# Optimization experiments

Hardware: AMD Instinct MI355X
Metric: run time of the kernel (lower is better)

Reference implementation:

```python
import jax, jax.numpy as jnp
import numpy as np


def setup_inputs() -> dict:
    key = jax.random.key(0)
    ks = jax.random.split(key, 6)
    b, t, k, h = 2, 2048, 256, 8
    s = 1.0 / np.sqrt(k)
    return {
        "x": jax.random.normal(ks[0], (b, t, k), dtype=jnp.float32),
        "Wq": jax.random.normal(ks[1], (k, k * h), dtype=jnp.float32) * s,
        "Wk": jax.random.normal(ks[2], (k, k * h), dtype=jnp.float32) * s,
        "Wv": jax.random.normal(ks[3], (k, k * h), dtype=jnp.float32) * s,
        "Wu": jax.random.normal(ks[4], (k * h, k), dtype=jnp.float32) * (1.0 / np.sqrt(k * h)),
        "bu": jnp.zeros((k,), dtype=jnp.float32),
    }


def reference(x, Wq, Wk, Wv, Wu, bu):
    b, t, k = x.shape
    h = Wq.shape[1] // k
    scale = k ** (-0.25)
    # projections -> [b, t, h, k] -> [b, h, t, k]
    q = (x @ Wq).reshape(b, t, h, k).transpose(0, 2, 1, 3) * scale
    kk = (x @ Wk).reshape(b, t, h, k).transpose(0, 2, 1, 3) * scale
    v = (x @ Wv).reshape(b, t, h, k).transpose(0, 2, 1, 3)
    dot = jnp.einsum('bhqk,bhsk->bhqs', q, kk)  # [b,h,t,t]
    attn = jax.nn.softmax(dot, axis=-1)
    out = jnp.einsum('bhqs,bhsk->bhqk', attn, v)  # [b,h,t,k]
    out = out.transpose(0, 2, 1, 3).reshape(b, t, h * k)
    return out @ Wu + bu
```

## Files before the change

kernel.cpp:

```cpp
#include <hip/hip_runtime.h>

using bf16x8   = __bf16 __attribute__((ext_vector_type(8)));
using floatx4  = float __attribute__((ext_vector_type(4)));
using floatx16 = float __attribute__((ext_vector_type(16)));

static __device__ __forceinline__ unsigned short f2b(float x) {
  unsigned u = __builtin_bit_cast(unsigned, x);
  u = (u + 0x7fffu + ((u >> 16) & 1u)) >> 16;
  return (unsigned short)u;
}

static __device__ __forceinline__ void gl_lds16(const unsigned short* g, unsigned short* l) {
  __builtin_amdgcn_global_load_lds((const __attribute__((address_space(1))) void*)g,
                                   (__attribute__((address_space(3))) void*)l, 16, 0, 0);
}

__global__ __launch_bounds__(256) void prep_kernel(const float* __restrict__ x,
                                                   const float* __restrict__ Wq,
                                                   const float* __restrict__ Wk,
                                                   const float* __restrict__ Wv,
                                                   const float* __restrict__ Wu,
                                                   unsigned short* __restrict__ xb,
                                                   unsigned short* __restrict__ wqkt,
                                                   unsigned short* __restrict__ wvt,
                                                   unsigned short* __restrict__ wut) {
  int bx = blockIdx.x;
  if (bx < 1024) {
    int i = (bx * 256 + threadIdx.x) * 4;
    float4 v = *(const float4*)(x + i);
    unsigned long long p = (unsigned long long)f2b(v.x) |
                           ((unsigned long long)f2b(v.y) << 16) |
                           ((unsigned long long)f2b(v.z) << 32) |
                           ((unsigned long long)f2b(v.w) << 48);
    *(unsigned long long*)(xb + i) = p;
    return;
  }
  __shared__ unsigned short T[64][65];
  const float* src;
  unsigned short* dst;
  int R, C, tile;
  if (bx < 1152)      { src = Wq; dst = wqkt;          R = 256;  C = 2048; tile = bx - 1024; }
  else if (bx < 1280) { src = Wk; dst = wqkt + 524288; R = 256;  C = 2048; tile = bx - 1152; }
  else if (bx < 1408) { src = Wv; dst = wvt;           R = 256;  C = 2048; tile = bx - 1280; }
  else                { src = Wu; dst = wut;           R = 2048; C = 256;  tile = bx - 1408; }
  int ctiles = C >> 6;
  int cx = tile % ctiles, ry = tile / ctiles;
  int r0 = ry * 64, c0 = cx * 64;
  int t = threadIdx.x;
#pragma unroll
  for (int i = 0; i < 16; ++i) {
    int idx = i * 256 + t;
    int r = idx >> 6, c = idx & 63;
    T[r][c] = f2b(src[(size_t)(r0 + r) * C + c0 + c]);
  }
  __syncthreads();
#pragma unroll
  for (int i = 0; i < 16; ++i) {
    int idx = i * 256 + t;
    int c = idx >> 6, r = idx & 63;
    dst[(size_t)(c0 + c) * R + r0 + r] = T[r][c];
  }
}

__global__ __launch_bounds__(256) void proj_kernel(const unsigned short* __restrict__ A,
                                                   const unsigned short* __restrict__ Bt,
                                                   unsigned short* __restrict__ qkb,
                                                   unsigned short* __restrict__ vtb) {
  __shared__ __align__(16) unsigned short SMEM[128 * 136];
  unsigned short* As = SMEM;
  unsigned short* Bs = SMEM + 4096;
  const int Kt = 256;
  int tid = threadIdx.x, lane = tid & 63, w = tid >> 6;
  int m16 = lane & 15, quad = lane >> 4;
  int wr = w & 1, wc = w >> 1;
  int m0 = blockIdx.y * 128, n0 = blockIdx.x * 128;
  int srow0 = w * 32 + (lane >> 2);
  int schunk = (lane & 3) ^ ((lane >> 2) & 3);
  floatx4 acc[4][4] = {};
  for (int k0 = 0; k0 < Kt; k0 += 32) {
    __syncthreads();
#pragma unroll
    for (int j = 0; j < 2; ++j) {
      int r = srow0 + j * 16;
      gl_lds16(A + (size_t)(m0 + r) * Kt + k0 + schunk * 8, &As[(w * 32 + j * 16) * 32]);
      gl_lds16(Bt + (size_t)(n0 + r) * Kt + k0 + schunk * 8, &Bs[(w * 32 + j * 16) * 32]);
    }
    __syncthreads();
    int sw = (quad ^ (m16 & 3)) * 8;
    bf16x8 af[4], bfr[4];
#pragma unroll
    for (int i = 0; i < 4; ++i) {
      af[i]  = *(const bf16x8*)(&As[(wr * 64 + i * 16 + m16) * 32 + sw]);
      bfr[i] = *(const bf16x8*)(&Bs[(wc * 64 + i * 16 + m16) * 32 + sw]);
    }
#pragma unroll
    for (int i = 0; i < 4; ++i)
#pragma unroll
      for (int jn = 0; jn < 4; ++jn)
        acc[i][jn] = __builtin_amdgcn_mfma_f32_16x16x32_bf16(af[i], bfr[jn], acc[i][jn], 0, 0, 0);
  }
  if (n0 < 4096) {
#pragma unroll
    for (int i = 0; i < 4; ++i)
#pragma unroll
      for (int jn = 0; jn < 4; ++jn)
#pragma unroll
        for (int r = 0; r < 4; ++r) {
          int m = m0 + wr * 64 + i * 16 + quad * 4 + r;
          int n = n0 + wc * 64 + jn * 16 + m16;
          qkb[(size_t)m * 4096 + n] = f2b(acc[i][jn][r]);
        }
  } else {
    __syncthreads();
    unsigned short* Vt = SMEM;
#pragma unroll
    for (int i = 0; i < 4; ++i)
#pragma unroll
      for (int jn = 0; jn < 4; ++jn)
#pragma unroll
        for (int r = 0; r < 4; ++r) {
          int nn = wc * 64 + jn * 16 + m16;
          int mm = wr * 64 + i * 16 + quad * 4 + r;
          Vt[nn * 136 + mm] = f2b(acc[i][jn][r]);
        }
    __syncthreads();
    int bb = m0 >> 11, t0 = m0 & 2047;
#pragma unroll
    for (int i2 = 0; i2 < 8; ++i2) {
      int idx = i2 * 256 + tid;
      int nn = idx >> 4;
      int mc = (idx & 15) * 8;
      uint4 v = *(const uint4*)(&Vt[nn * 136 + mc]);
      *(uint4*)(&vtb[((size_t)(bb * 2048 + n0 - 4096 + nn)) * 2048 + t0 + mc]) = v;
    }
  }
}

__global__ __launch_bounds__(256) void out_kernel(const unsigned short* __restrict__ A,
                                                  const unsigned short* __restrict__ Bt,
                                                  float* __restrict__ Cout,
                                                  const float* __restrict__ bias) {
  __shared__ unsigned short As[64 * 128];
  __shared__ unsigned short Bs[64 * 128];
  const int Kt = 2048;
  int tid = threadIdx.x, lane = tid & 63, w = tid >> 6;
  int m16 = lane & 15, quad = lane >> 4;
  int m0 = blockIdx.y * 64, n0 = blockIdx.x * 64;
  int srow_i = lane >> 4;
  int spos = lane & 15;
  int rsw = m16 & 7;
  floatx4 acc[4] = {};
  for (int k0 = 0; k0 < Kt; k0 += 128) {
    __syncthreads();
#pragma unroll
    for (int j = 0; j < 4; ++j) {
      int r = w * 16 + j * 4 + srow_i;
      gl_lds16(A + (size_t)(m0 + r) * Kt + k0 + ((spos ^ (r & 7)) * 8), &As[(w * 16 + j * 4) * 128]);
      gl_lds16(Bt + (size_t)(n0 + r) * Kt + k0 + ((spos ^ (r & 7)) * 8), &Bs[(w * 16 + j * 4) * 128]);
    }
    __syncthreads();
    bf16x8 af[4];
#pragma unroll
    for (int kk = 0; kk < 4; ++kk)
      af[kk] = *(const bf16x8*)(&As[(w * 16 + m16) * 128 + (((kk * 4 + quad) ^ rsw) * 8)]);
#pragma unroll
    for (int nt = 0; nt < 4; ++nt)
#pragma unroll
      for (int kk = 0; kk < 4; ++kk) {
        bf16x8 bfv = *(const bf16x8*)(&Bs[(nt * 16 + m16) * 128 + (((kk * 4 + quad) ^ rsw) * 8)]);
        acc[nt] = __builtin_amdgcn_mfma_f32_16x16x32_bf16(af[kk], bfv, acc[nt], 0, 0, 0);
      }
  }
#pragma unroll
  for (int nt = 0; nt < 4; ++nt)
#pragma unroll
    for (int r = 0; r < 4; ++r) {
      int m = m0 + w * 16 + quad * 4 + r;
      int n = n0 + nt * 16 + m16;
      Cout[(size_t)m * 256 + n] = acc[nt][r] + bias[n];
    }
}

__global__ __launch_bounds__(512, 2) void attn_kernel(const unsigned short* __restrict__ qk,
                                                      const unsigned short* __restrict__ vt,
                                                      unsigned short* __restrict__ ao) {
  __shared__ __align__(16) unsigned char SM[150016];
  unsigned short* KsBuf = (unsigned short*)SM;
  unsigned short* VsBuf = (unsigned short*)(SM + 65536);
  float* lsh = (float*)(SM + 149504);
  int tid = threadIdx.x, lane = tid & 63, w = tid >> 6;
  int c32 = lane & 31, hi = lane >> 5;
  int qg = w & 3, u = w >> 2;
  unsigned short* Pw = (unsigned short*)(SM + 131072) + w * 1152;
  int id = blockIdx.x;
  int xcd = id & 7, j = id >> 3;
  int bh = xcd + 8 * (j & 1);
  int q0 = (j >> 1) * 128;
  int b = bh >> 3, h = bh & 7;

  bf16x8 qf[16];
  const unsigned short* qrow =
      qk + (size_t)(b * 2048 + q0 + qg * 32 + c32) * 4096 + h * 256 + hi * 8;
#pragma unroll
  for (int kk = 0; kk < 16; ++kk) qf[kk] = *(const bf16x8*)(qrow + kk * 16);

  floatx16 O[8] = {};
  float lacc = 0.f;

  const unsigned short* kbase = qk + (size_t)b * 2048 * 4096 + 2048 + h * 256;
  const unsigned short* vbase = vt + (size_t)bh * 256 * 2048;

  int krow_i = lane >> 5, kpos = lane & 31;
  int vrow_i = lane >> 3, vpos = lane & 7;
  int ksw = c32 & 7;

#pragma unroll
  for (int i = 0; i < 4; ++i) {
    int kr = i * 2 + krow_i;
    gl_lds16(kbase + (size_t)(w * 8 + kr) * 4096 + ((kpos ^ (kr & 7)) * 8),
             KsBuf + (w * 8 + i * 2) * 256);
    int vr = i * 8 + vrow_i;
    gl_lds16(vbase + (size_t)(w * 32 + vr) * 2048 + ((vpos ^ vrow_i) * 8),
             VsBuf + (w * 32 + i * 8) * 64);
  }

  for (int st = 0; st < 32; ++st) {
    int cur = st & 1;
    unsigned short* Kc = KsBuf + cur * 16384;
    unsigned short* Vc = VsBuf + cur * 16384;
    __syncthreads();
    if (st < 31) {
      int s0 = (st + 1) * 64;
      unsigned short* kd = KsBuf + (1 - cur) * 16384;
      unsigned short* vd = VsBuf + (1 - cur) * 16384;
#pragma unroll
      for (int i = 0; i < 4; ++i) {
        int kr = i * 2 + krow_i;
        gl_lds16(kbase + (size_t)(s0 + w * 8 + kr) * 4096 + ((kpos ^ (kr & 7)) * 8),
                 kd + (w * 8 + i * 2) * 256);
        int vr = i * 8 + vrow_i;
        gl_lds16(vbase + (size_t)(w * 32 + vr) * 2048 + s0 + ((vpos ^ vrow_i) * 8),
                 vd + (w * 32 + i * 8) * 64);
      }
    }

    floatx16 s = {};
    const unsigned short* krl = Kc + (u * 32 + c32) * 256;
#pragma unroll
    for (int kk = 0; kk < 16; ++kk) {
      bf16x8 kf = *(const bf16x8*)(krl + (((kk * 2 + hi) ^ ksw) * 8));
      s = __builtin_amdgcn_mfma_f32_32x32x16_bf16(kf, qf[kk], s, 0, 0, 0);
    }
    float lsum = 0.f;
#pragma unroll
    for (int i = 0; i < 16; ++i) {
      float p = __expf(s[i] * 0.0625f);
      lsum += p;
      int sl = (i & 3) + 8 * (i >> 2) + 4 * hi;
      Pw[c32 * 36 + sl] = f2b(p);
    }
    lacc += lsum;
    bf16x8 paf[2];
#pragma unroll
    for (int f = 0; f < 2; ++f) paf[f] = *(const bf16x8*)(Pw + c32 * 36 + f * 16 + hi * 8);
#pragma unroll
    for (int dt = 0; dt < 8; ++dt) {
      const unsigned short* vrl = Vc + (dt * 32 + c32) * 64;
#pragma unroll
      for (int f = 0; f < 2; ++f) {
        bf16x8 vf = *(const bf16x8*)(vrl + (((u * 4 + f * 2 + hi) ^ ksw) * 8));
        O[dt] = __builtin_amdgcn_mfma_f32_32x32x16_bf16(paf[f], vf, O[dt], 0, 0, 0);
      }
    }
  }

  float lw = lacc + __shfl_xor(lacc, 32);
  __syncthreads();
  float* osh = (float*)SM;
  if (u == 0) {
    float* od = osh + qg * 8192;
#pragma unroll
    for (int dt = 0; dt < 8; ++dt)
#pragma unroll
      for (int i = 0; i < 16; ++i) {
        int q = (i & 3) + 8 * (i >> 2) + 4 * hi;
        od[q * 256 + dt * 32 + c32] = O[dt][i];
      }
    if (hi == 0) lsh[qg * 32 + c32] = lw;
  }
  __syncthreads();
  if (u == 1 && hi == 0) lsh[qg * 32 + c32] += lw;
  __syncthreads();
  if (u == 1) {
    float* od = osh + qg * 8192;
    unsigned short* aor = ao + (size_t)(b * 2048 + q0 + qg * 32) * 2048 + h * 256;
#pragma unroll
    for (int i = 0; i < 16; ++i) {
      int q = (i & 3) + 8 * (i >> 2) + 4 * hi;
      float lr = 1.0f / lsh[qg * 32 + q];
#pragma unroll
      for (int dt = 0; dt < 8; ++dt) {
        float v = (O[dt][i] + od[q * 256 + dt * 32 + c32]) * lr;
        aor[(size_t)q * 2048 + dt * 32 + c32] = f2b(v);
      }
    }
  }
}

extern "C" void kernel_launch(void* const* d_in, const int* in_sizes, int n_in,
                              void* d_out, int out_size, void* d_ws, size_t ws_size,
                              hipStream_t stream) {
  const float* x  = (const float*)d_in[0];
  const float* Wq = (const float*)d_in[1];
  const float* Wk = (const float*)d_in[2];
  const float* Wv = (const float*)d_in[3];
  const float* Wu = (const float*)d_in[4];
  const float* bu = (const float*)d_in[5];

  unsigned short* xb   = (unsigned short*)d_ws;
  unsigned short* wqkt = xb + 1048576;
  unsigned short* wvt  = wqkt + 1048576;
  unsigned short* wut  = wvt + 524288;
  unsigned short* qkb  = wut + 524288;
  unsigned short* vtb  = qkb + 16777216;
  unsigned short* aob  = vtb + 8388608;

  prep_kernel<<<1536, 256, 0, stream>>>(x, Wq, Wk, Wv, Wu, xb, wqkt, wvt, wut);
  proj_kernel<<<dim3(48, 32), 256, 0, stream>>>(xb, wqkt, qkb, vtb);
  attn_kernel<<<256, 512, 0, stream>>>(qkb, vtb, aob);
  out_kernel<<<dim3(4, 64), 256, 0, stream>>>(aob, wut, (float*)d_out, bu);
}
```

Baseline: 201.3 us.

## Halve attention block to four waves, each computing two query groups per K fragment

The attention kernel now uses 256 threads where each wave handles two 32-row query groups, reusing each K and V fragment read from shared memory for two MFMAs. This is meant to cut the LDS read traffic per MFMA. The softmax scale is folded into the Q projection epilogue, and P values are written as packed 64-bit stores instead of scalar shorts. In exchange each wave holds twice the accumulators and Q fragments, raising register pressure, and each block has half as many waves to hide latency.

```diff
diff --git a/kernel.cpp b/kernel.cpp
--- a/kernel.cpp
+++ b/kernel.cpp
@@ -100,6 +100,7 @@
         acc[i][jn] = __builtin_amdgcn_mfma_f32_16x16x32_bf16(af[i], bfr[jn], acc[i][jn], 0, 0, 0);
   }
   if (n0 < 4096) {
+    float qscale = (n0 < 2048) ? 0.0625f : 1.0f;
 #pragma unroll
     for (int i = 0; i < 4; ++i)
 #pragma unroll
@@ -108,7 +109,7 @@
         for (int r = 0; r < 4; ++r) {
           int m = m0 + wr * 64 + i * 16 + quad * 4 + r;
           int n = n0 + wc * 64 + jn * 16 + m16;
-          qkb[(size_t)m * 4096 + n] = f2b(acc[i][jn][r]);
+          qkb[(size_t)m * 4096 + n] = f2b(acc[i][jn][r] * qscale);
         }
   } else {
     __syncthreads();
@@ -181,31 +182,34 @@
     }
 }
 
-__global__ __launch_bounds__(512, 2) void attn_kernel(const unsigned short* __restrict__ qk,
+__global__ __launch_bounds__(256, 1) void attn_kernel(const unsigned short* __restrict__ qk,
                                                       const unsigned short* __restrict__ vt,
                                                       unsigned short* __restrict__ ao) {
-  __shared__ __align__(16) unsigned char SM[150016];
+  __shared__ __align__(16) unsigned char SM[150528];
   unsigned short* KsBuf = (unsigned short*)SM;
   unsigned short* VsBuf = (unsigned short*)(SM + 65536);
   float* lsh = (float*)(SM + 149504);
   int tid = threadIdx.x, lane = tid & 63, w = tid >> 6;
   int c32 = lane & 31, hi = lane >> 5;
-  int qg = w & 3, u = w >> 2;
-  unsigned short* Pw = (unsigned short*)(SM + 131072) + w * 1152;
+  int qsub = w & 1, u = w >> 1;
+  unsigned short* Pw = (unsigned short*)(SM + 131072) + w * 2304;
   int id = blockIdx.x;
   int xcd = id & 7, j = id >> 3;
   int bh = xcd + 8 * (j & 1);
   int q0 = (j >> 1) * 128;
   int b = bh >> 3, h = bh & 7;
 
-  bf16x8 qf[16];
-  const unsigned short* qrow =
-      qk + (size_t)(b * 2048 + q0 + qg * 32 + c32) * 4096 + h * 256 + hi * 8;
-#pragma unroll
-  for (int kk = 0; kk < 16; ++kk) qf[kk] = *(const bf16x8*)(qrow + kk * 16);
-
-  floatx16 O[8] = {};
-  float lacc = 0.f;
+  bf16x8 qf[2][16];
+#pragma unroll
+  for (int qg = 0; qg < 2; ++qg) {
+    const unsigned short* qrow =
+        qk + (size_t)(b * 2048 + q0 + qsub * 64 + qg * 32 + c32) * 4096 + h * 256 + hi * 8;
+#pragma unroll
+    for (int kk = 0; kk < 16; ++kk) qf[qg][kk] = *(const bf16x8*)(qrow + kk * 16);
+  }
+
+  floatx16 O[2][8] = {};
+  float lacc[2] = {0.f, 0.f};
 
   const unsigned short* kbase = qk + (size_t)b * 2048 * 4096 + 2048 + h * 256;
   const unsigned short* vbase = vt + (size_t)bh * 256 * 2048;
@@ -215,13 +219,13 @@
   int ksw = c32 & 7;
 
 #pragma unroll
-  for (int i = 0; i < 4; ++i) {
+  for (int i = 0; i < 8; ++i) {
     int kr = i * 2 + krow_i;
-    gl_lds16(kbase + (size_t)(w * 8 + kr) * 4096 + ((kpos ^ (kr & 7)) * 8),
-             KsBuf + (w * 8 + i * 2) * 256);
+    gl_lds16(kbase + (size_t)(w * 16 + kr) * 4096 + ((kpos ^ (kr & 7)) * 8),
+             KsBuf + (w * 16 + i * 2) * 256);
     int vr = i * 8 + vrow_i;
-    gl_lds16(vbase + (size_t)(w * 32 + vr) * 2048 + ((vpos ^ vrow_i) * 8),
-             VsBuf + (w * 32 + i * 8) * 64);
+    gl_lds16(vbase + (size_t)(w * 64 + vr) * 2048 + ((vpos ^ vrow_i) * 8),
+             VsBuf + (w * 64 + i * 8) * 64);
   }
 
   for (int st = 0; st < 32; ++st) {
@@ -234,76 +238,101 @@
       unsigned short* kd = KsBuf + (1 - cur) * 16384;
       unsigned short* vd = VsBuf + (1 - cur) * 16384;
 #pragma unroll
-      for (int i = 0; i < 4; ++i) {
+      for (int i = 0; i < 8; ++i) {
         int kr = i * 2 + krow_i;
-        gl_lds16(kbase + (size_t)(s0 + w * 8 + kr) * 4096 + ((kpos ^ (kr & 7)) * 8),
-                 kd + (w * 8 + i * 2) * 256);
+        gl_lds16(kbase + (size_t)(s0 + w * 16 + kr) * 4096 + ((kpos ^ (kr & 7)) * 8),
+                 kd + (w * 16 + i * 2) * 256);
         int vr = i * 8 + vrow_i;
-        gl_lds16(vbase + (size_t)(w * 32 + vr) * 2048 + s0 + ((vpos ^ vrow_i) * 8),
-                 vd + (w * 32 + i * 8) * 64);
-      }
-    }
-
-    floatx16 s = {};
+        gl_lds16(vbase + (size_t)(w * 64 + vr) * 2048 + s0 + ((vpos ^ vrow_i) * 8),
+                 vd + (w * 64 + i * 8) * 64);
+      }
+    }
+
+    floatx16 s0v = {}, s1v = {};
     const unsigned short* krl = Kc + (u * 32 + c32) * 256;
 #pragma unroll
     for (int kk = 0; kk < 16; ++kk) {
       bf16x8 kf = *(const bf16x8*)(krl + (((kk * 2 + hi) ^ ksw) * 8));
-      s = __builtin_amdgcn_mfma_f32_32x32x16_bf16(kf, qf[kk], s, 0, 0, 0);
-    }
-    float lsum = 0.f;
-#pragma unroll
-    for (int i = 0; i < 16; ++i) {
-      float p = __expf(s[i] * 0.0625f);
-      lsum += p;
-      int sl = (i & 3) + 8 * (i >> 2) + 4 * hi;
-      Pw[c32 * 36 + sl] = f2b(p);
-    }
-    lacc += lsum;
-    bf16x8 paf[2];
-#pragma unroll
-    for (int f = 0; f < 2; ++f) paf[f] = *(const bf16x8*)(Pw + c32 * 36 + f * 16 + hi * 8);
+      s0v = __builtin_amdgcn_mfma_f32_32x32x16_bf16(kf, qf[0][kk], s0v, 0, 0, 0);
+      s1v = __builtin_amdgcn_mfma_f32_32x32x16_bf16(kf, qf[1][kk], s1v, 0, 0, 0);
+    }
+#pragma unroll
+    for (int qg = 0; qg < 2; ++qg) {
+      const floatx16& sv = qg ? s1v : s0v;
+      unsigned short* Pq = Pw + qg * 1152;
+      float ls = 0.f;
+#pragma unroll
+      for (int g = 0; g < 4; ++g) {
+        float p0 = __expf(sv[g * 4 + 0]);
+        float p1 = __expf(sv[g * 4 + 1]);
+        float p2 = __expf(sv[g * 4 + 2]);
+        float p3 = __expf(sv[g * 4 + 3]);
+        ls += p0 + p1 + p2 + p3;
+        unsigned long long pk = (unsigned long long)f2b(p0) |
+                                ((unsigned long long)f2b(p1) << 16) |
+                                ((unsigned long long)f2b(p2) << 32) |
+                                ((unsigned long long)f2b(p3) << 48);
+        *(unsigned long long*)(Pq + c32 * 36 + g * 8 + hi * 4) = pk;
+      }
+      lacc[qg] += ls;
+    }
+    bf16x8 paf[2][2];
+#pragma unroll
+    for (int qg = 0; qg < 2; ++qg)
+#pragma unroll
+      for (int f = 0; f < 2; ++f)
+        paf[qg][f] = *(const bf16x8*)(Pw + qg * 1152 + c32 * 36 + f * 16 + hi * 8);
 #pragma unroll
     for (int dt = 0; dt < 8; ++dt) {
       const unsigned short* vrl = Vc + (dt * 32 + c32) * 64;
 #pragma unroll
       for (int f = 0; f < 2; ++f) {
         bf16x8 vf = *(const bf16x8*)(vrl + (((u * 4 + f * 2 + hi) ^ ksw) * 8));
-        O[dt] = __builtin_amdgcn_mfma_f32_32x32x16_bf16(paf[f], vf, O[dt], 0, 0, 0);
-      }
-    }
-  }
-
-  float lw = lacc + __shfl_xor(lacc, 32);
+        O[0][dt] = __builtin_amdgcn_mfma_f32_32x32x16_bf16(paf[0][f], vf, O[0][dt], 0, 0, 0);
+        O[1][dt] = __builtin_amdgcn_mfma_f32_32x32x16_bf16(paf[1][f], vf, O[1][dt], 0, 0, 0);
+      }
+    }
+  }
+
+  float lw[2];
+#pragma unroll
+  for (int qg = 0; qg < 2; ++qg) lw[qg] = lacc[qg] + __shfl_xor(lacc[qg], 32);
   __syncthreads();
   float* osh = (float*)SM;
   if (u == 0) {
-    float* od = osh + qg * 8192;
-#pragma unroll
-    for (int dt = 0; dt < 8; ++dt)
-#pragma unroll
-      for (int i = 0; i < 16; ++i) {
-        int q = (i & 3) + 8 * (i >> 2) + 4 * hi;
-        od[q * 256 + dt * 32 + c32] = O[dt][i];
-      }
-    if (hi == 0) lsh[qg * 32 + c32] = lw;
-  }
-  __syncthreads();
-  if (u == 1 && hi == 0) lsh[qg * 32 + c32] += lw;
+    float* od = osh + qsub * 16384;
+#pragma unroll
+    for (int qg = 0; qg < 2; ++qg)
+#pragma unroll
+      for (int dt = 0; dt < 8; ++dt)
+#pragma unroll
+        for (int i = 0; i < 16; ++i) {
+          int ql = (i & 3) + 8 * (i >> 2) + 4 * hi;
+          od[(qg * 32 + ql) * 256 + dt * 32 + c32] = O[qg][dt][i];
+        }
+  }
+  if (hi == 0) {
+#pragma unroll
+    for (int qg = 0; qg < 2; ++qg)
+      lsh[u * 128 + qsub * 64 + qg * 32 + c32] = lw[qg];
+  }
   __syncthreads();
   if (u == 1) {
-    float* od = osh + qg * 8192;
-    unsigned short* aor = ao + (size_t)(b * 2048 + q0 + qg * 32) * 2048 + h * 256;
-#pragma unroll
-    for (int i = 0; i < 16; ++i) {
-      int q = (i & 3) + 8 * (i >> 2) + 4 * hi;
-      float lr = 1.0f / lsh[qg * 32 + q];
-#pragma unroll
-      for (int dt = 0; dt < 8; ++dt) {
-        float v = (O[dt][i] + od[q * 256 + dt * 32 + c32]) * lr;
-        aor[(size_t)q * 2048 + dt * 32 + c32] = f2b(v);
-      }
-    }
+    float* od = osh + qsub * 16384;
+    unsigned short* aor = ao + (size_t)(b * 2048 + q0 + qsub * 64) * 2048 + h * 256;
+#pragma unroll
+    for (int qg = 0; qg < 2; ++qg)
+#pragma unroll
+      for (int i = 0; i < 16; ++i) {
+        int ql = (i & 3) + 8 * (i >> 2) + 4 * hi;
+        int q = qg * 32 + ql;
+        float lr = 1.0f / (lsh[qsub * 64 + q] + lsh[128 + qsub * 64 + q]);
+#pragma unroll
+        for (int dt = 0; dt < 8; ++dt) {
+          float v = (O[qg][dt][i] + od[q * 256 + dt * 32 + c32]) * lr;
+          aor[(size_t)q * 2048 + dt * 32 + c32] = f2b(v);
+        }
+      }
   }
 }
 
@@ -327,6 +356,6 @@
 
   prep_kernel<<<1536, 256, 0, stream>>>(x, Wq, Wk, Wv, Wu, xb, wqkt, wvt, wut);
   proj_kernel<<<dim3(48, 32), 256, 0, stream>>>(xb, wqkt, qkb, vtb);
-  attn_kernel<<<256, 512, 0, stream>>>(qkb, vtb, aob);
+  attn_kernel<<<256, 256, 0, stream>>>(qkb, vtb, aob);
   out_kernel<<<dim3(4, 64), 256, 0, stream>>>(aob, wut, (float*)d_out, bu);
 }
```

After: 258.1 us. 28.2% more time.
